# Performance work log

Hardware: AMD Instinct MI355X
Metric: run time of the kernel (lower is better)

## Reference

```python
import jax, jax.numpy as jnp
import numpy as np

N_HEAD = 16
LORA_RANK = 16
ROPE_BASE = 10000.0


def _rope_cos_sin(T, D, dtype):
    # GPT-NeoX style rotate-half RoPE tables, shape [T, D]
    inv_freq = 1.0 / (ROPE_BASE ** (jnp.arange(0, D, 2, dtype=jnp.float32) / D))
    t = jnp.arange(T, dtype=jnp.float32)
    freqs = t[:, None] * inv_freq[None, :]          # [T, D/2]
    emb = jnp.concatenate([freqs, freqs], axis=-1)   # [T, D]
    return jnp.cos(emb).astype(dtype), jnp.sin(emb).astype(dtype)


def _rotate_half(x):
    x1, x2 = jnp.split(x, 2, axis=-1)
    return jnp.concatenate([-x2, x1], axis=-1)


def _apply_rope(q, k, cos, sin):
    # q,k: [B,H,T,D]; cos,sin: [T,D]
    c = cos[None, None, :, :]
    s = sin[None, None, :, :]
    return q * c + _rotate_half(q) * s, k * c + _rotate_half(k) * s


def setup_inputs() -> dict:
    key = jax.random.key(0)
    ks = jax.random.split(key, 6)
    B, T, C = 4, 1024, 2048
    r = LORA_RANK
    sc = 1.0 / np.sqrt(C)
    return {
        "x": jax.random.normal(ks[0], (B, T, C), jnp.float32),
        "qkvo_delta": jax.random.normal(ks[1], (B, 8 * r, C), jnp.float32) * 0.02,
        "Wq": jax.random.normal(ks[2], (C, C), jnp.float32) * sc,
        "Wk": jax.random.normal(ks[3], (C, C), jnp.float32) * sc,
        "Wv": jax.random.normal(ks[4], (C, C), jnp.float32) * sc,
        "Wo": jax.random.normal(ks[5], (C, C), jnp.float32) * sc,
    }


def reference(x, qkvo_delta, Wq, Wk, Wv, Wo):
    B, T, C = x.shape
    H = N_HEAD
    D = C // H

    # split LoRA deltas: each [B, r, C]
    dqA, dqB, dkA, dkB, dvA, dvB, doA, doB = jnp.split(qkvo_delta, 8, axis=1)

    def merged(W, dB, dA):
        # W [out,in] + dB^T @ dA -> [B, out, in]
        return W[None] + jnp.einsum('bro,bri->boi', dB, dA)

    def proj(inp, Wm):
        # inp @ Wm^T (per-batch merged weight)
        return jnp.einsum('bti,boi->bto', inp, Wm)

    q = proj(x, merged(Wq, dqB, dqA))
    k = proj(x, merged(Wk, dkB, dkA))
    v = proj(x, merged(Wv, dvB, dvA))

    # [B,T,C] -> [B,H,T,D]
    def heads(t):
        return t.reshape(B, T, H, D).transpose(0, 2, 1, 3)

    q, k, v = heads(q), heads(k), heads(v)

    cos, sin = _rope_cos_sin(T, D, x.dtype)
    q, k = _apply_rope(q, k, cos, sin)

    # full (non-causal) SDPA, matching is_causal=False in the source
    scale = 1.0 / np.sqrt(D)
    scores = jnp.einsum('bhtd,bhsd->bhts', q, k) * scale
    attn = jax.nn.softmax(scores, axis=-1)
    y = jnp.einsum('bhts,bhsd->bhtd', attn, v)

    y = y.transpose(0, 2, 1, 3).reshape(B, T, C)
    out = proj(y, merged(Wo, doB, doA))
    return out
```

## Files before the change

kernel.cpp:

```cpp
#include <hip/hip_runtime.h>
#include <cstdint>
#include <cstddef>

typedef __attribute__((ext_vector_type(8))) __bf16 bf8_t;
typedef __attribute__((ext_vector_type(8))) short s8_t;
typedef __attribute__((ext_vector_type(4))) short s4_t;
typedef __attribute__((ext_vector_type(4))) float f4_t;

__device__ __forceinline__ float bf2f(unsigned short h) {
  union { unsigned u; float f; } v; v.u = (unsigned)h << 16; return v.f;
}
__device__ __forceinline__ unsigned short f2bf(float f) {
  union { float f; unsigned u; } v; v.f = f;
  return (unsigned short)((v.u + 0x7FFFu + ((v.u >> 16) & 1u)) >> 16);
}

#define GL16(gp, lp) __builtin_amdgcn_global_load_lds( \
    (__attribute__((address_space(1))) void*)(gp),     \
    (__attribute__((address_space(3))) void*)(lp), 16, 0, 0)

struct ConvArgs {
  const float* src[6];
  unsigned short* dst[6];
  int n4[6];
  int thr[5];
};
__global__ void k_conv_all(ConvArgs a) {
  int blk = blockIdx.x, seg = 0;
#pragma unroll
  for (int s = 0; s < 5; ++s) seg += (blk >= a.thr[s]);
  int base = (seg == 0) ? 0 : a.thr[seg - 1];
  int i = (blk - base) * 256 + threadIdx.x;
  if (i >= a.n4[seg]) return;
  float4 v = reinterpret_cast<const float4*>(a.src[seg])[i];
  s4_t o;
  o.x = (short)f2bf(v.x); o.y = (short)f2bf(v.y);
  o.z = (short)f2bf(v.z); o.w = (short)f2bf(v.w);
  reinterpret_cast<s4_t*>(a.dst[seg])[i] = o;
}

__global__ void k_rope_table(float* __restrict__ cosT, float* __restrict__ sinT) {
  int t = blockIdx.x, d = threadIdx.x;
  float inv = exp2f(-(float)d * (13.287712379549449f / 64.0f));
  float ang = (float)t * inv;
  cosT[t * 64 + d] = cosf(ang);
  sinT[t * 64 + d] = sinf(ang);
}

#define UOFF 262144
__global__ __launch_bounds__(256) void k_lora_mfma(
    const unsigned short* __restrict__ X,
    const unsigned short* __restrict__ dlb,
    float* __restrict__ u, int pstart, int pcount) {
  __shared__ __align__(16) unsigned short Xs[64 * 64];
  __shared__ __align__(16) unsigned short Da[64 * 64];
  const int t = threadIdx.x;
  const int b = blockIdx.y;
  const int z = blockIdx.z;
  const int m0 = blockIdx.x * 64;
  const int w = t >> 6, lane = t & 63, lr = lane & 15, lg = lane >> 4;
  const int nrow = pcount * 16;
  f4_t acc[4] = {};
  for (int k0 = z * 512; k0 < z * 512 + 512; k0 += 64) {
    __syncthreads();
#pragma unroll
    for (int i = 0; i < 2; ++i) {
      int idx = i * 256 + t;
      int row = idx >> 3, c = idx & 7;
      GL16(X + ((size_t)b * 1024 + m0 + row) * 2048 + k0 + ((c ^ (row & 7)) * 8),
           Xs + (size_t)idx * 8);
      int ric = row < nrow ? row : nrow - 1;
      int g = (pstart + (ric >> 4)) * 32 + (ric & 15);
      GL16(dlb + ((size_t)b * 128 + g) * 2048 + k0 + ((c ^ (ric & 7)) * 8),
           Da + (size_t)idx * 8);
    }
    __syncthreads();
#pragma unroll
    for (int kk = 0; kk < 2; ++kk) {
      bf8_t af = *(const bf8_t*)&Xs[(w * 16 + lr) * 64 + (((kk * 4 + lg) ^ (lr & 7)) * 8)];
#pragma unroll
      for (int n = 0; n < 4; ++n) {
        if (n < pcount) {
          bf8_t bfv = *(const bf8_t*)&Da[(n * 16 + lr) * 64 + (((kk * 4 + lg) ^ (lr & 7)) * 8)];
          acc[n] = __builtin_amdgcn_mfma_f32_16x16x32_bf16(af, bfv, acc[n], 0, 0, 0);
        }
      }
    }
  }
#pragma unroll
  for (int n = 0; n < 4; ++n) {
    if (n < pcount) {
#pragma unroll
      for (int j = 0; j < 4; ++j)
        u[(size_t)z * UOFF +
          (((size_t)b * 4 + pstart + n) * 16 + lr) * 1024 + m0 + w * 16 + lg * 4 + j] = acc[n][j];
    }
  }
}

struct GArgs {
  const unsigned short *Bw0, *Bw1, *Bw2;
  void *o0, *o1, *o2;
  int m0_, m1_, m2_;
  int p0_, p1_, p2_;
};
#define BM 128
#define BN 128
#define BKK 64
__global__ __launch_bounds__(256, 2) void k_gemm(
    const unsigned short* __restrict__ A,
    GArgs ga,
    const float* __restrict__ u,
    const float* __restrict__ dl) {
  constexpr int K = 2048;
  const int z = blockIdx.z;
  const unsigned short* Bw = z == 0 ? ga.Bw0 : (z == 1 ? ga.Bw1 : ga.Bw2);
  void* outv = z == 0 ? ga.o0 : (z == 1 ? ga.o1 : ga.o2);
  const int mode = z == 0 ? ga.m0_ : (z == 1 ? ga.m1_ : ga.m2_);
  const int p = z == 0 ? ga.p0_ : (z == 1 ? ga.p1_ : ga.p2_);
  __shared__ unsigned short As[BM * BKK];
  __shared__ unsigned short Bs[BN * BKK];
  const int t = threadIdx.x;
  const int lin = (int)blockIdx.x + ((int)blockIdx.y << 4);
  const int xcd = lin & 7, rnk = lin >> 3;
  const int m0 = (((xcd >> 1) << 3) | (rnk >> 3)) * BM;
  const int n0 = (((xcd & 1) << 3) | (rnk & 7)) * BN;
  const int lane = t & 63;
  const int w = t >> 6;
  const int wr = (w >> 1) * 64, wc = (w & 1) * 64;
  const int lr = lane & 15;
  const int lg = lane >> 4;
  const int srow = t >> 3;
  const int sdst = (t & 7) * 8;
  const int ssrc = ((t & 7) ^ (srow & 7)) * 8;
  f4_t acc[4][4] = {};

  for (int k0 = 0; k0 < K; k0 += BKK) {
#pragma unroll
    for (int j = 0; j < 4; ++j) {
      int row = j * 32 + srow;
      GL16(A  + (size_t)(m0 + row) * K + k0 + ssrc, As + row * BKK + sdst);
      GL16(Bw + (size_t)(n0 + row) * K + k0 + ssrc, Bs + row * BKK + sdst);
    }
    __syncthreads();
#pragma unroll
    for (int kk = 0; kk < 2; ++kk) {
      bf8_t af[4], bfr[4];
#pragma unroll
      for (int m = 0; m < 4; ++m) {
        int row_ = wr + m * 16 + lr;
        af[m] = *(const bf8_t*)&As[row_ * BKK + (((kk * 4 + lg) ^ (lr & 7)) * 8)];
      }
#pragma unroll
      for (int n = 0; n < 4; ++n) {
        int row_ = wc + n * 16 + lr;
        bfr[n] = *(const bf8_t*)&Bs[row_ * BKK + (((kk * 4 + lg) ^ (lr & 7)) * 8)];
      }
#pragma unroll
      for (int m = 0; m < 4; ++m)
#pragma unroll
        for (int n = 0; n < 4; ++n)
          acc[m][n] = __builtin_amdgcn_mfma_f32_16x16x32_bf16(af[m], bfr[n], acc[m][n], 0, 0, 0);
    }
    __syncthreads();
  }

  const int b = m0 >> 10;
  const int t0r = m0 & 1023;
  for (int idx = t; idx < 128 * 32; idx += 256) {
    int rr = idx >> 5, r = idx & 31;
    float val = 0.0f;
    if (r < 16) {
      size_t ub = (((size_t)b * 4 + p) * 16 + r) * 1024 + t0r + rr;
      val = (u[ub] + u[UOFF + ub]) + (u[2 * UOFF + ub] + u[3 * UOFF + ub]);
    }
    As[rr * 32 + r] = f2bf(val);
  }
  for (int idx = t; idx < 128 * 32; idx += 256) {
    int cc = idx >> 5, r = idx & 31;
    float val = (r < 16) ? dl[((size_t)b * 128 + p * 32 + 16 + r) * 2048 + n0 + cc] : 0.0f;
    Bs[cc * 32 + r] = f2bf(val);
  }
  __syncthreads();
  {
    bf8_t af[4], bfr[4];
#pragma unroll
    for (int m = 0; m < 4; ++m)
      af[m] = *(const bf8_t*)&As[(wr + m * 16 + lr) * 32 + lg * 8];
#pragma unroll
    for (int n = 0; n < 4; ++n)
      bfr[n] = *(const bf8_t*)&Bs[(wc + n * 16 + lr) * 32 + lg * 8];
#pragma unroll
    for (int m = 0; m < 4; ++m)
#pragma unroll
      for (int n = 0; n < 4; ++n)
        acc[m][n] = __builtin_amdgcn_mfma_f32_16x16x32_bf16(af[m], bfr[n], acc[m][n], 0, 0, 0);
  }

  unsigned short* out16 = (unsigned short*)outv;
  float* out32 = (float*)outv;
#pragma unroll
  for (int m = 0; m < 4; ++m) {
    int ri = wr + m * 16 + lg * 4;
#pragma unroll
    for (int j = 0; j < 4; ++j) {
      int grow = m0 + ri + j;
      int gb = grow >> 10, gt = grow & 1023;
#pragma unroll
      for (int n = 0; n < 4; ++n) {
        int gcol = n0 + wc + n * 16 + lr;
        float fv = acc[m][n][j];
        if (mode == 0) {
          size_t dst = (((size_t)gb * 16 + (gcol >> 7)) * 1024 + gt) * 128 + (gcol & 127);
          out16[dst] = f2bf(fv);
        } else if (mode == 1) {
          size_t dst = (((size_t)gb * 16 + (gcol >> 7)) * 128 + (gcol & 127)) * 1024 + gt;
          out16[dst] = f2bf(fv);
        } else {
          out32[(size_t)grow * 2048 + gcol] = fv;
        }
      }
    }
  }
}

__global__ void k_rope(unsigned short* __restrict__ X,
                       const float* __restrict__ cosT, const float* __restrict__ sinT) {
  int idx = blockIdx.x * 256 + threadIdx.x;
  int d0 = (idx & 7) * 8;
  int tt = (idx >> 3) & 1023;
  size_t base = (size_t)(idx >> 3) * 128 + d0;
  s8_t a = *(s8_t*)&X[base];
  s8_t bb = *(s8_t*)&X[base + 64];
  float4 c0 = *(const float4*)&cosT[tt * 64 + d0];
  float4 c1 = *(const float4*)&cosT[tt * 64 + d0 + 4];
  float4 sv0 = *(const float4*)&sinT[tt * 64 + d0];
  float4 sv1 = *(const float4*)&sinT[tt * 64 + d0 + 4];
  float cv[8] = {c0.x, c0.y, c0.z, c0.w, c1.x, c1.y, c1.z, c1.w};
  float sw[8] = {sv0.x, sv0.y, sv0.z, sv0.w, sv1.x, sv1.y, sv1.z, sv1.w};
  s8_t ra, rb;
#pragma unroll
  for (int j = 0; j < 8; ++j) {
    float av = bf2f((unsigned short)a[j]);
    float bv = bf2f((unsigned short)bb[j]);
    ra[j] = (short)f2bf(av * cv[j] - bv * sw[j]);
    rb[j] = (short)f2bf(bv * cv[j] + av * sw[j]);
  }
  *(s8_t*)&X[base] = ra;
  *(s8_t*)&X[base + 64] = rb;
}

__global__ __launch_bounds__(512, 4) void k_attn(
    const unsigned short* __restrict__ Qg,
    const unsigned short* __restrict__ Kg,
    const unsigned short* __restrict__ Vt,
    const float* __restrict__ cosT,
    const float* __restrict__ sinT,
    unsigned short* __restrict__ Y) {
  const float scale = 0.08838834764831845f;
  const float L2E = 1.4426950408889634f;
  const float C1 = scale * L2E;
  const float C2 = 12.0f * L2E;
  const int bid = blockIdx.x;
  const int wg = (bid & 7) * 64 + (bid >> 3);
  const int bh = wg >> 3;
  const int b = bh >> 4, h = bh & 15;
  const int t = threadIdx.x;
  const int w = t >> 6, lane = t & 63;
  const int lr = lane & 15, lg = lane >> 4;
  const int q0 = (wg & 7) * 128 + w * 16;
  const unsigned short* Q  = Qg + (size_t)bh * 131072;
  const unsigned short* Kp = Kg + (size_t)bh * 131072;
  const unsigned short* Vp = Vt + (size_t)bh * 131072;
  __shared__ __align__(16) unsigned short Ks[64 * 128];
  __shared__ __align__(16) unsigned short Vs[128 * 64];
  __shared__ __align__(16) unsigned short Ps[8][16 * 72];
  unsigned short* Pw = Ps[w];

  s8_t one_s;
#pragma unroll
  for (int e = 0; e < 8; ++e) one_s[e] = (short)0x3F80;
  const bf8_t ones = *(bf8_t*)&one_s;

  bf8_t qf[4];
  {
    s8_t qs[4];
#pragma unroll
    for (int kk = 0; kk < 4; ++kk)
      qs[kk] = *(const s8_t*)&Q[(size_t)(q0 + lr) * 128 + kk * 32 + lg * 8];
    const float* ct = cosT + (size_t)(q0 + lr) * 64 + lg * 8;
    const float* st = sinT + (size_t)(q0 + lr) * 64 + lg * 8;
    float4 cl0 = *(const float4*)ct,        cl1 = *(const float4*)(ct + 4);
    float4 ch0 = *(const float4*)(ct + 32), ch1 = *(const float4*)(ct + 36);
    float4 sl0 = *(const float4*)st,        sl1 = *(const float4*)(st + 4);
    float4 sh0 = *(const float4*)(st + 32), sh1 = *(const float4*)(st + 36);
    float cl[8] = {cl0.x, cl0.y, cl0.z, cl0.w, cl1.x, cl1.y, cl1.z, cl1.w};
    float ch[8] = {ch0.x, ch0.y, ch0.z, ch0.w, ch1.x, ch1.y, ch1.z, ch1.w};
    float sl[8] = {sl0.x, sl0.y, sl0.z, sl0.w, sl1.x, sl1.y, sl1.z, sl1.w};
    float sh[8] = {sh0.x, sh0.y, sh0.z, sh0.w, sh1.x, sh1.y, sh1.z, sh1.w};
    s8_t r0, r1, r2, r3;
#pragma unroll
    for (int e = 0; e < 8; ++e) {
      float x0 = bf2f((unsigned short)qs[0][e]);
      float x1 = bf2f((unsigned short)qs[1][e]);
      float x2 = bf2f((unsigned short)qs[2][e]);
      float x3 = bf2f((unsigned short)qs[3][e]);
      r0[e] = (short)f2bf(x0 * cl[e] - x2 * sl[e]);
      r1[e] = (short)f2bf(x1 * ch[e] - x3 * sh[e]);
      r2[e] = (short)f2bf(x2 * cl[e] + x0 * sl[e]);
      r3[e] = (short)f2bf(x3 * ch[e] + x1 * sh[e]);
    }
    qf[0] = *(bf8_t*)&r0; qf[1] = *(bf8_t*)&r1;
    qf[2] = *(bf8_t*)&r2; qf[3] = *(bf8_t*)&r3;
  }

  f4_t o[8] = {};
  f4_t lacc = {};

  auto ldK = [&](int s0, int i) {
    int idx = i * 512 + t, s = idx >> 4, c = t & 15;
    return *(const s8_t*)&Kp[(size_t)(s0 + s) * 128 + ((c ^ (s & 7)) * 8)];
  };
  auto ldV = [&](int s0, int i) {
    int idx = i * 512 + t, d = idx >> 3, c = t & 7;
    return *(const s8_t*)&Vp[(size_t)d * 1024 + s0 + ((c ^ (d & 7)) * 8)];
  };
  s8_t kr0 = ldK(0, 0), kr1 = ldK(0, 1), vr0 = ldV(0, 0), vr1 = ldV(0, 1);

  for (int s0 = 0; s0 < 1024; s0 += 64) {
    __builtin_amdgcn_s_barrier();
    *(s8_t*)&Ks[((size_t)t) * 8]        = kr0;
    *(s8_t*)&Ks[((size_t)512 + t) * 8]  = kr1;
    *(s8_t*)&Vs[((size_t)t) * 8]        = vr0;
    *(s8_t*)&Vs[((size_t)512 + t) * 8]  = vr1;
    int sn = (s0 < 960) ? s0 + 64 : 0;
    kr0 = ldK(sn, 0); kr1 = ldK(sn, 1); vr0 = ldV(sn, 0); vr1 = ldV(sn, 1);
    asm volatile("s_waitcnt lgkmcnt(0)" ::: "memory");
    __builtin_amdgcn_s_barrier();

    f4_t sf[4];
    __builtin_amdgcn_s_setprio(1);
#pragma unroll
    for (int ss = 0; ss < 4; ++ss) {
      f4_t c = {0.0f, 0.0f, 0.0f, 0.0f};
#pragma unroll
      for (int kk = 0; kk < 4; ++kk) {
        bf8_t kf = *(const bf8_t*)&Ks[(ss * 16 + lr) * 128 + (((kk * 4 + lg) ^ (lr & 7)) * 8)];
        c = __builtin_amdgcn_mfma_f32_16x16x32_bf16(kf, qf[kk], c, 0, 0, 0);
      }
      sf[ss] = c;
    }
    __builtin_amdgcn_s_setprio(0);
#pragma unroll
    for (int ss = 0; ss < 4; ++ss) {
      float p0 = exp2f(sf[ss][0] * C1 - C2);
      float p1 = exp2f(sf[ss][1] * C1 - C2);
      float p2 = exp2f(sf[ss][2] * C1 - C2);
      float p3 = exp2f(sf[ss][3] * C1 - C2);
      unsigned lo, hi;
      asm("v_cvt_pk_bf16_f32 %0, %1, %2" : "=v"(lo) : "v"(p0), "v"(p1));
      asm("v_cvt_pk_bf16_f32 %0, %1, %2" : "=v"(hi) : "v"(p2), "v"(p3));
      unsigned pk2[2] = {lo, hi};
      *(s4_t*)&Pw[lr * 72 + ss * 16 + lg * 4] = *(s4_t*)pk2;
    }
    bf8_t pa0 = *(const bf8_t*)&Pw[lr * 72 + lg * 8];
    bf8_t pa1 = *(const bf8_t*)&Pw[lr * 72 + 32 + lg * 8];
    __builtin_amdgcn_s_setprio(1);
#pragma unroll
    for (int n = 0; n < 8; ++n) {
      int d = n * 16 + lr;
      bf8_t v0 = *(const bf8_t*)&Vs[d * 64 + (((0 + lg) ^ (lr & 7)) * 8)];
      bf8_t v1 = *(const bf8_t*)&Vs[d * 64 + (((4 + lg) ^ (lr & 7)) * 8)];
      o[n] = __builtin_amdgcn_mfma_f32_16x16x32_bf16(pa0, v0, o[n], 0, 0, 0);
      o[n] = __builtin_amdgcn_mfma_f32_16x16x32_bf16(pa1, v1, o[n], 0, 0, 0);
    }
    lacc = __builtin_amdgcn_mfma_f32_16x16x32_bf16(pa0, ones, lacc, 0, 0, 0);
    lacc = __builtin_amdgcn_mfma_f32_16x16x32_bf16(pa1, ones, lacc, 0, 0, 0);
    __builtin_amdgcn_s_setprio(0);
  }

  float linv[4];
#pragma unroll
  for (int j = 0; j < 4; ++j) linv[j] = 1.0f / lacc[j];
#pragma unroll
  for (int n = 0; n < 8; ++n)
#pragma unroll
    for (int j = 0; j < 4; ++j) {
      int qg = q0 + lg * 4 + j;
      Y[((size_t)b * 1024 + qg) * 2048 + h * 128 + n * 16 + lr] =
          f2bf(o[n][j] * linv[j]);
    }
}

extern "C" void kernel_launch(void* const* d_in, const int* in_sizes, int n_in,
                              void* d_out, int out_size, void* d_ws, size_t ws_size,
                              hipStream_t stream) {
  const float* x  = (const float*)d_in[0];
  const float* dl = (const float*)d_in[1];
  const float* W[4] = {(const float*)d_in[2], (const float*)d_in[3],
                       (const float*)d_in[4], (const float*)d_in[5]};
  char* ws = (char*)d_ws;
  size_t off = 0;
  auto take = [&](size_t bytes) {
    void* p = ws + off; off += (bytes + 255) & ~(size_t)255; return p;
  };
  unsigned short* xb = (unsigned short*)take(8388608ull * 2);
  unsigned short* Wb[4];
  for (int i = 0; i < 4; ++i) Wb[i] = (unsigned short*)take(4194304ull * 2);
  unsigned short* qb = (unsigned short*)take(8388608ull * 2);
  unsigned short* kb = (unsigned short*)take(8388608ull * 2);
  unsigned short* vT = (unsigned short*)take(8388608ull * 2);
  unsigned short* y  = (unsigned short*)take(8388608ull * 2);
  float* u    = (float*)take(4ull * UOFF * 4);
  float* cosT = (float*)take(1024ull * 64 * 4);
  float* sinT = (float*)take(1024ull * 64 * 4);
  unsigned short* dlb = (unsigned short*)take(1048576ull * 2);
  if (off > ws_size) return;

  ConvArgs ca;
  ca.src[0] = x;  ca.dst[0] = xb;  ca.n4[0] = 2097152;
  for (int i = 0; i < 4; ++i) { ca.src[1 + i] = W[i]; ca.dst[1 + i] = Wb[i]; ca.n4[1 + i] = 1048576; }
  ca.src[5] = dl; ca.dst[5] = dlb; ca.n4[5] = 262144;
  ca.thr[0] = 8192; ca.thr[1] = 12288; ca.thr[2] = 16384; ca.thr[3] = 20480; ca.thr[4] = 24576;
  k_conv_all<<<25600, 256, 0, stream>>>(ca);
  k_rope_table<<<1024, 64, 0, stream>>>(cosT, sinT);
  k_lora_mfma<<<dim3(16, 4, 4), 256, 0, stream>>>(xb, dlb, u, 0, 3);

  GArgs gq;
  gq.Bw0 = Wb[0]; gq.o0 = qb;    gq.m0_ = 0; gq.p0_ = 0;
  gq.Bw1 = Wb[1]; gq.o1 = kb;    gq.m1_ = 0; gq.p1_ = 1;
  gq.Bw2 = Wb[2]; gq.o2 = vT;    gq.m2_ = 1; gq.p2_ = 2;
  k_gemm<<<dim3(16, 32, 3), 256, 0, stream>>>(xb, gq, u, dl);

  k_rope<<<2048, 256, 0, stream>>>(kb, cosT, sinT);
  k_attn<<<512, 512, 0, stream>>>(qb, kb, vT, cosT, sinT, y);
  k_lora_mfma<<<dim3(16, 4, 4), 256, 0, stream>>>(y, dlb, u, 3, 1);

  GArgs go;
  go.Bw0 = Wb[3]; go.o0 = d_out; go.m0_ = 2; go.p0_ = 3;
  go.Bw1 = Wb[3]; go.o1 = d_out; go.m1_ = 2; go.p1_ = 3;
  go.Bw2 = Wb[3]; go.o2 = d_out; go.m2_ = 2; go.p2_ = 3;
  k_gemm<<<dim3(16, 32, 1), 256, 0, stream>>>(y, go, u, dl);
}
```

Before: 306.3 us.

## Process two query row-blocks per wave in attention to reuse K/V fragments

The attention kernel now uses 4 waves of 256 threads per block instead of 8, with each wave handling 32 query rows (two 16-row tiles) rather than 16. Each K and V fragment read from LDS feeds two MFMAs, which halves LDS read traffic per unit of compute. Each thread issues twice as many global K/V loads per tile. The trade-off is more registers per thread (doubled accumulators and Q fragments) and fewer waves per block, which may lower occupancy and latency hiding.

```diff
diff --git a/kernel.cpp b/kernel.cpp
--- a/kernel.cpp
+++ b/kernel.cpp
@@ -250,7 +250,7 @@
   *(s8_t*)&X[base + 64] = rb;
 }
 
-__global__ __launch_bounds__(512, 4) void k_attn(
+__global__ __launch_bounds__(256, 2) void k_attn(
     const unsigned short* __restrict__ Qg,
     const unsigned short* __restrict__ Kg,
     const unsigned short* __restrict__ Vt,
@@ -268,13 +268,13 @@
   const int t = threadIdx.x;
   const int w = t >> 6, lane = t & 63;
   const int lr = lane & 15, lg = lane >> 4;
-  const int q0 = (wg & 7) * 128 + w * 16;
+  const int q0 = (wg & 7) * 128 + w * 32;
   const unsigned short* Q  = Qg + (size_t)bh * 131072;
   const unsigned short* Kp = Kg + (size_t)bh * 131072;
   const unsigned short* Vp = Vt + (size_t)bh * 131072;
   __shared__ __align__(16) unsigned short Ks[64 * 128];
   __shared__ __align__(16) unsigned short Vs[128 * 64];
-  __shared__ __align__(16) unsigned short Ps[8][16 * 72];
+  __shared__ __align__(16) unsigned short Ps[4][32 * 72];
   unsigned short* Pw = Ps[w];
 
   s8_t one_s;
@@ -282,14 +282,16 @@
   for (int e = 0; e < 8; ++e) one_s[e] = (short)0x3F80;
   const bf8_t ones = *(bf8_t*)&one_s;
 
-  bf8_t qf[4];
-  {
+  bf8_t qf[2][4];
+#pragma unroll
+  for (int qr = 0; qr < 2; ++qr) {
+    int qrow = q0 + qr * 16 + lr;
     s8_t qs[4];
 #pragma unroll
     for (int kk = 0; kk < 4; ++kk)
-      qs[kk] = *(const s8_t*)&Q[(size_t)(q0 + lr) * 128 + kk * 32 + lg * 8];
-    const float* ct = cosT + (size_t)(q0 + lr) * 64 + lg * 8;
-    const float* st = sinT + (size_t)(q0 + lr) * 64 + lg * 8;
+      qs[kk] = *(const s8_t*)&Q[(size_t)qrow * 128 + kk * 32 + lg * 8];
+    const float* ct = cosT + (size_t)qrow * 64 + lg * 8;
+    const float* st = sinT + (size_t)qrow * 64 + lg * 8;
     float4 cl0 = *(const float4*)ct,        cl1 = *(const float4*)(ct + 4);
     float4 ch0 = *(const float4*)(ct + 32), ch1 = *(const float4*)(ct + 36);
     float4 sl0 = *(const float4*)st,        sl1 = *(const float4*)(st + 4);
@@ -310,86 +312,106 @@
       r2[e] = (short)f2bf(x2 * cl[e] + x0 * sl[e]);
       r3[e] = (short)f2bf(x3 * ch[e] + x1 * sh[e]);
     }
-    qf[0] = *(bf8_t*)&r0; qf[1] = *(bf8_t*)&r1;
-    qf[2] = *(bf8_t*)&r2; qf[3] = *(bf8_t*)&r3;
-  }
-
-  f4_t o[8] = {};
-  f4_t lacc = {};
+    qf[qr][0] = *(bf8_t*)&r0; qf[qr][1] = *(bf8_t*)&r1;
+    qf[qr][2] = *(bf8_t*)&r2; qf[qr][3] = *(bf8_t*)&r3;
+  }
+
+  f4_t o[2][8] = {};
+  f4_t lacc[2] = {};
 
   auto ldK = [&](int s0, int i) {
-    int idx = i * 512 + t, s = idx >> 4, c = t & 15;
+    int idx = i * 256 + t, s = idx >> 4, c = idx & 15;
     return *(const s8_t*)&Kp[(size_t)(s0 + s) * 128 + ((c ^ (s & 7)) * 8)];
   };
   auto ldV = [&](int s0, int i) {
-    int idx = i * 512 + t, d = idx >> 3, c = t & 7;
+    int idx = i * 256 + t, d = idx >> 3, c = idx & 7;
     return *(const s8_t*)&Vp[(size_t)d * 1024 + s0 + ((c ^ (d & 7)) * 8)];
   };
-  s8_t kr0 = ldK(0, 0), kr1 = ldK(0, 1), vr0 = ldV(0, 0), vr1 = ldV(0, 1);
+  s8_t kr[4], vr[4];
+#pragma unroll
+  for (int i = 0; i < 4; ++i) { kr[i] = ldK(0, i); vr[i] = ldV(0, i); }
 
   for (int s0 = 0; s0 < 1024; s0 += 64) {
     __builtin_amdgcn_s_barrier();
-    *(s8_t*)&Ks[((size_t)t) * 8]        = kr0;
-    *(s8_t*)&Ks[((size_t)512 + t) * 8]  = kr1;
-    *(s8_t*)&Vs[((size_t)t) * 8]        = vr0;
-    *(s8_t*)&Vs[((size_t)512 + t) * 8]  = vr1;
+#pragma unroll
+    for (int i = 0; i < 4; ++i) {
+      *(s8_t*)&Ks[((size_t)(i * 256 + t)) * 8] = kr[i];
+      *(s8_t*)&Vs[((size_t)(i * 256 + t)) * 8] = vr[i];
+    }
     int sn = (s0 < 960) ? s0 + 64 : 0;
-    kr0 = ldK(sn, 0); kr1 = ldK(sn, 1); vr0 = ldV(sn, 0); vr1 = ldV(sn, 1);
+#pragma unroll
+    for (int i = 0; i < 4; ++i) { kr[i] = ldK(sn, i); vr[i] = ldV(sn, i); }
     asm volatile("s_waitcnt lgkmcnt(0)" ::: "memory");
     __builtin_amdgcn_s_barrier();
 
-    f4_t sf[4];
+    f4_t sf[2][4];
     __builtin_amdgcn_s_setprio(1);
 #pragma unroll
     for (int ss = 0; ss < 4; ++ss) {
-      f4_t c = {0.0f, 0.0f, 0.0f, 0.0f};
+      f4_t c0 = {0.0f, 0.0f, 0.0f, 0.0f};
+      f4_t c1 = {0.0f, 0.0f, 0.0f, 0.0f};
 #pragma unroll
       for (int kk = 0; kk < 4; ++kk) {
         bf8_t kf = *(const bf8_t*)&Ks[(ss * 16 + lr) * 128 + (((kk * 4 + lg) ^ (lr & 7)) * 8)];
-        c = __builtin_amdgcn_mfma_f32_16x16x32_bf16(kf, qf[kk], c, 0, 0, 0);
-      }
-      sf[ss] = c;
+        c0 = __builtin_amdgcn_mfma_f32_16x16x32_bf16(kf, qf[0][kk], c0, 0, 0, 0);
+        c1 = __builtin_amdgcn_mfma_f32_16x16x32_bf16(kf, qf[1][kk], c1, 0, 0, 0);
+      }
+      sf[0][ss] = c0; sf[1][ss] = c1;
     }
     __builtin_amdgcn_s_setprio(0);
 #pragma unroll
-    for (int ss = 0; ss < 4; ++ss) {
-      float p0 = exp2f(sf[ss][0] * C1 - C2);
-      float p1 = exp2f(sf[ss][1] * C1 - C2);
-      float p2 = exp2f(sf[ss][2] * C1 - C2);
-      float p3 = exp2f(sf[ss][3] * C1 - C2);
-      unsigned lo, hi;
-      asm("v_cvt_pk_bf16_f32 %0, %1, %2" : "=v"(lo) : "v"(p0), "v"(p1));
-      asm("v_cvt_pk_bf16_f32 %0, %1, %2" : "=v"(hi) : "v"(p2), "v"(p3));
-      unsigned pk2[2] = {lo, hi};
-      *(s4_t*)&Pw[lr * 72 + ss * 16 + lg * 4] = *(s4_t*)pk2;
-    }
-    bf8_t pa0 = *(const bf8_t*)&Pw[lr * 72 + lg * 8];
-    bf8_t pa1 = *(const bf8_t*)&Pw[lr * 72 + 32 + lg * 8];
+    for (int qr = 0; qr < 2; ++qr)
+#pragma unroll
+      for (int ss = 0; ss < 4; ++ss) {
+        float p0 = exp2f(sf[qr][ss][0] * C1 - C2);
+        float p1 = exp2f(sf[qr][ss][1] * C1 - C2);
+        float p2 = exp2f(sf[qr][ss][2] * C1 - C2);
+        float p3 = exp2f(sf[qr][ss][3] * C1 - C2);
+        unsigned lo, hi;
+        asm("v_cvt_pk_bf16_f32 %0, %1, %2" : "=v"(lo) : "v"(p0), "v"(p1));
+        asm("v_cvt_pk_bf16_f32 %0, %1, %2" : "=v"(hi) : "v"(p2), "v"(p3));
+        unsigned pk2[2] = {lo, hi};
+        *(s4_t*)&Pw[(qr * 16 + lr) * 72 + ss * 16 + lg * 4] = *(s4_t*)pk2;
+      }
+    bf8_t pa[2][2];
+#pragma unroll
+    for (int qr = 0; qr < 2; ++qr) {
+      pa[qr][0] = *(const bf8_t*)&Pw[(qr * 16 + lr) * 72 + lg * 8];
+      pa[qr][1] = *(const bf8_t*)&Pw[(qr * 16 + lr) * 72 + 32 + lg * 8];
+    }
     __builtin_amdgcn_s_setprio(1);
 #pragma unroll
     for (int n = 0; n < 8; ++n) {
       int d = n * 16 + lr;
       bf8_t v0 = *(const bf8_t*)&Vs[d * 64 + (((0 + lg) ^ (lr & 7)) * 8)];
       bf8_t v1 = *(const bf8_t*)&Vs[d * 64 + (((4 + lg) ^ (lr & 7)) * 8)];
-      o[n] = __builtin_amdgcn_mfma_f32_16x16x32_bf16(pa0, v0, o[n], 0, 0, 0);
-      o[n] = __builtin_amdgcn_mfma_f32_16x16x32_bf16(pa1, v1, o[n], 0, 0, 0);
-    }
-    lacc = __builtin_amdgcn_mfma_f32_16x16x32_bf16(pa0, ones, lacc, 0, 0, 0);
-    lacc = __builtin_amdgcn_mfma_f32_16x16x32_bf16(pa1, ones, lacc, 0, 0, 0);
+      o[0][n] = __builtin_amdgcn_mfma_f32_16x16x32_bf16(pa[0][0], v0, o[0][n], 0, 0, 0);
+      o[0][n] = __builtin_amdgcn_mfma_f32_16x16x32_bf16(pa[0][1], v1, o[0][n], 0, 0, 0);
+      o[1][n] = __builtin_amdgcn_mfma_f32_16x16x32_bf16(pa[1][0], v0, o[1][n], 0, 0, 0);
+      o[1][n] = __builtin_amdgcn_mfma_f32_16x16x32_bf16(pa[1][1], v1, o[1][n], 0, 0, 0);
+    }
+#pragma unroll
+    for (int qr = 0; qr < 2; ++qr) {
+      lacc[qr] = __builtin_amdgcn_mfma_f32_16x16x32_bf16(pa[qr][0], ones, lacc[qr], 0, 0, 0);
+      lacc[qr] = __builtin_amdgcn_mfma_f32_16x16x32_bf16(pa[qr][1], ones, lacc[qr], 0, 0, 0);
+    }
     __builtin_amdgcn_s_setprio(0);
   }
 
-  float linv[4];
-#pragma unroll
-  for (int j = 0; j < 4; ++j) linv[j] = 1.0f / lacc[j];
-#pragma unroll
-  for (int n = 0; n < 8; ++n)
-#pragma unroll
-    for (int j = 0; j < 4; ++j) {
-      int qg = q0 + lg * 4 + j;
-      Y[((size_t)b * 1024 + qg) * 2048 + h * 128 + n * 16 + lr] =
-          f2bf(o[n][j] * linv[j]);
-    }
+#pragma unroll
+  for (int qr = 0; qr < 2; ++qr) {
+    float linv[4];
+#pragma unroll
+    for (int j = 0; j < 4; ++j) linv[j] = 1.0f / lacc[qr][j];
+#pragma unroll
+    for (int n = 0; n < 8; ++n)
+#pragma unroll
+      for (int j = 0; j < 4; ++j) {
+        int qg = q0 + qr * 16 + lg * 4 + j;
+        Y[((size_t)b * 1024 + qg) * 2048 + h * 128 + n * 16 + lr] =
+            f2bf(o[qr][n][j] * linv[j]);
+      }
+  }
 }
 
 extern "C" void kernel_launch(void* const* d_in, const int* in_sizes, int n_in,
@@ -433,7 +455,7 @@
   k_gemm<<<dim3(16, 32, 3), 256, 0, stream>>>(xb, gq, u, dl);
 
   k_rope<<<2048, 256, 0, stream>>>(kb, cosT, sinT);
-  k_attn<<<512, 512, 0, stream>>>(qb, kb, vT, cosT, sinT, y);
+  k_attn<<<512, 256, 0, stream>>>(qb, kb, vT, cosT, sinT, y);
   k_lora_mfma<<<dim3(16, 4, 4), 256, 0, stream>>>(y, dlb, u, 3, 1);
 
   GArgs go;
```

Result: no change. 305.9 us (-0.1%).
